# Performance work log

Measured on AMD Instinct MI355X. Metric: run time of the kernel, lower is better.

## Reference

```python
import jax, jax.numpy as jnp
import numpy as np

B, T, E = 2, 2048, 2048
H, H_KV, D = 16, 8, 128
THETA = 10000.0


def setup_inputs() -> dict:
    key = jax.random.key(0)
    ks = jax.random.split(key, 5)
    s = lambda n: (1.0 / np.sqrt(n))
    x = jax.random.normal(ks[0], (B, T, E), dtype=jnp.float32)
    wq = jax.random.normal(ks[1], (E, H * D), dtype=jnp.float32) * s(E)
    wk = jax.random.normal(ks[2], (E, H_KV * D), dtype=jnp.float32) * s(E)
    wv = jax.random.normal(ks[3], (E, H_KV * D), dtype=jnp.float32) * s(E)
    wo = jax.random.normal(ks[4], (H * D, E), dtype=jnp.float32) * s(H * D)
    # causal mask, broadcast over batch and heads
    mask = jnp.tril(jnp.ones((T, T), dtype=jnp.int32))[None, None, :, :]
    return {"x": x, "mask": mask, "wq": wq, "wk": wk, "wv": wv, "wo": wo}


def _rope(q, k):
    # q,k: [B,H,T,D]; deinterleave even/odd, rotate, concat halves (as in source)
    Tq, Dh = q.shape[2], q.shape[3] // 2
    inv = 1.0 / (THETA ** (jnp.arange(Dh, dtype=jnp.float32) / Dh))
    ang = jnp.arange(Tq, dtype=jnp.float32)[:, None] * inv[None, :]  # [T,Dh]
    c, s = jnp.cos(ang), jnp.sin(ang)  # broadcast over [B,H]
    q1, q2 = q[..., ::2], q[..., 1::2]
    k1, k2 = k[..., ::2], k[..., 1::2]
    q_rot = jnp.concatenate([q1 * c - q2 * s, q2 * c + q1 * s], axis=-1)
    k_rot = jnp.concatenate([k1 * c - k2 * s, k2 * c + k1 * s], axis=-1)
    return q_rot, k_rot


def reference(x, mask, wq, wk, wv, wo):
    Bx, Tx, _ = x.shape
    scale = D ** -0.5
    q = (x @ wq).reshape(Bx, Tx, H, D).transpose(0, 2, 1, 3)      # [B,H,T,D]
    k = (x @ wk).reshape(Bx, Tx, H_KV, D).transpose(0, 2, 1, 3)   # [B,Hkv,T,D]
    v = (x @ wv).reshape(Bx, Tx, H_KV, D).transpose(0, 2, 1, 3)
    # torch .repeat tiles along head axis: [kv0..kv7, kv0..kv7]
    k = jnp.tile(k, (1, H // H_KV, 1, 1))
    v = jnp.tile(v, (1, H // H_KV, 1, 1))
    q, k = _rope(q, k)
    attn = jnp.einsum('bhtd,bhsd->bhts', q, k) * scale
    attn = jnp.where(mask == 0, -jnp.inf, attn)
    w = jax.nn.softmax(attn, axis=-1)
    w = jnp.where(jnp.isnan(w), 0.0, w)
    out = jnp.einsum('bhts,bhsd->bhtd', w, v)
    out = out.transpose(0, 2, 1, 3).reshape(Bx, Tx, H * D)
    return out @ wo
```

## Files before the change

### kernel.cpp

```cpp
#include <hip/hip_runtime.h>
#include <hip/hip_bf16.h>
#include <cstdint>

typedef short bf16x8 __attribute__((ext_vector_type(8)));
typedef float f32x4 __attribute__((ext_vector_type(4)));
typedef unsigned short u16;
typedef unsigned int u32;

#define TT 2048

__device__ __forceinline__ u16 f2bf(float f) {
    __hip_bfloat16 h = __float2bfloat16(f);
    return __builtin_bit_cast(u16, h);
}
__device__ __forceinline__ float bf2f(u16 u) {
    return __builtin_bit_cast(float, (u32)u << 16);
}
__device__ __forceinline__ f32x4 mfma16(bf16x8 a, bf16x8 b, f32x4 c) {
    return __builtin_amdgcn_mfma_f32_16x16x32_bf16(a, b, c, 0, 0, 0);
}
__device__ __forceinline__ bf16x8 ldg8(const u16* p) {
    return __builtin_bit_cast(bf16x8, *reinterpret_cast<const uint4*>(p));
}
__device__ __forceinline__ bf16x8 lds8(const u16* p) {
    return *reinterpret_cast<const bf16x8*>(p);
}
__device__ __forceinline__ void gll16(const u16* g, u16* l) {
    __builtin_amdgcn_global_load_lds(
        (const __attribute__((address_space(1))) void*)g,
        (__attribute__((address_space(3))) void*)l, 16, 0, 0);
}

#define ASMBAR asm volatile("s_barrier" ::: "memory")
#define WAIT_VM8 asm volatile("s_waitcnt vmcnt(8)" ::: "memory")
#define WAIT_VM0 asm volatile("s_waitcnt vmcnt(0)" ::: "memory")
#define WAIT_LGKM0 asm volatile("s_waitcnt lgkmcnt(0)" ::: "memory")

__global__ __launch_bounds__(256) void prologue(const float* __restrict__ x,
                                                const float* __restrict__ wq,
                                                const float* __restrict__ wk,
                                                const float* __restrict__ wv,
                                                const float* __restrict__ wo,
                                                u16* __restrict__ xb,
                                                u16* __restrict__ wqkvT,
                                                u16* __restrict__ woT) {
    const int z = blockIdx.z;
    const int tid = threadIdx.x;
    if (z == 4) {
        int bix = blockIdx.y * 32 + blockIdx.x;
#pragma unroll
        for (int k = 0; k < 4; k++) {
            int idx = (bix * 1024 + k * 256 + tid) * 8;
            float4 a = *reinterpret_cast<const float4*>(&x[idx]);
            float4 b = *reinterpret_cast<const float4*>(&x[idx + 4]);
            u16 o[8] = {f2bf(a.x), f2bf(a.y), f2bf(a.z), f2bf(a.w),
                        f2bf(b.x), f2bf(b.y), f2bf(b.z), f2bf(b.w)};
            *reinterpret_cast<uint4*>(&xb[idx]) = *reinterpret_cast<const uint4*>(o);
        }
        return;
    }
    const float* src;
    u16* dst;
    int C, rope;
    const int R = 2048;
    if (z == 0) { src = wq; dst = wqkvT;               C = 2048; rope = 1; }
    else if (z == 1) { src = wk; dst = wqkvT + 2048 * 2048; C = 1024; rope = 1; }
    else if (z == 2) { src = wv; dst = wqkvT + 3072 * 2048; C = 1024; rope = 0; }
    else { src = wo; dst = woT;                        C = 2048; rope = 0; }
    const int cb = blockIdx.x, rb = blockIdx.y;
    if (cb * 64 >= C) return;

    __shared__ float tl[64][65];
#pragma unroll
    for (int i = 0; i < 16; i++) {
        int li = i * 256 + tid;
        int tr = li >> 6, tc = li & 63;
        tl[tr][tc] = src[(size_t)(rb * 64 + tr) * C + cb * 64 + tc];
    }
    __syncthreads();
#pragma unroll
    for (int i = 0; i < 16; i++) {
        int li = i * 256 + tid;
        int dr = li >> 6, dc = li & 63;
        int c = cb * 64 + dr;
        int j;
        if (rope) {
            int head = c >> 7, cl = c & 127, ii = cl >> 1, odd = cl & 1;
            j = head * 128 + ((ii & 15) | (odd << 4) | ((ii >> 4) << 5));
        } else {
            j = c;
        }
        dst[(size_t)j * R + rb * 64 + dc] = f2bf(tl[dc][dr]);
    }
}

template <int MODE>
__global__ __launch_bounds__(512, 2) void gemm256(const u16* __restrict__ A,
                                                  const u16* __restrict__ BT,
                                                  void* __restrict__ P0, void* __restrict__ P1,
                                                  void* __restrict__ P2, int M, int N, int K) {
    __shared__ __align__(16) u16 smA[2][256 * 64];
    __shared__ __align__(16) u16 smB[2][256 * 64];
    const int tid = threadIdx.x;
    const int w = tid >> 6, lane = tid & 63, quad = lane >> 4, l15 = lane & 15;
    const int wr = w >> 2, wc = w & 3;
    const int bm = blockIdx.y, bn = blockIdx.x;

    f32x4 acc[8][4];
    const f32x4 zf = {0.f, 0.f, 0.f, 0.f};
#pragma unroll
    for (int i = 0; i < 8; i++)
#pragma unroll
        for (int j = 0; j < 4; j++) acc[i][j] = zf;

    const u16* aSrc[4];
    const u16* bSrc[4];
#pragma unroll
    for (int i = 0; i < 4; i++) {
        int o = i * 512 + tid;
        int r = o >> 3, p = o & 7;
        int cc = p ^ (r & 7);
        aSrc[i] = A + (size_t)(bm * 256 + r) * K + cc * 8;
        bSrc[i] = BT + (size_t)(bn * 256 + r) * K + cc * 8;
    }
    auto stage = [&](int buf) {
#pragma unroll
        for (int i = 0; i < 4; i++) {
            gll16(aSrc[i], &smA[buf][(i * 512 + w * 64) * 8]);
            aSrc[i] += 64;
        }
#pragma unroll
        for (int i = 0; i < 4; i++) {
            gll16(bSrc[i], &smB[buf][(i * 512 + w * 64) * 8]);
            bSrc[i] += 64;
        }
    };

    stage(0);
    stage(1);
    WAIT_VM8;
    ASMBAR;

    const int nkt = K >> 6;
    for (int kt = 0; kt < nkt; ++kt) {
        const int cur = kt & 1;
        bf16x8 a[4][2], b01[2][2], b23[2][2];
#pragma unroll
        for (int mi = 0; mi < 4; mi++)
#pragma unroll
            for (int ks = 0; ks < 2; ks++) {
                int row = wr * 128 + mi * 16 + l15, cd = ks * 4 + quad;
                a[mi][ks] = lds8(&smA[cur][row * 64 + ((cd ^ (row & 7)) * 8)]);
            }
#pragma unroll
        for (int ni = 0; ni < 2; ni++)
#pragma unroll
            for (int ks = 0; ks < 2; ks++) {
                int row = wc * 64 + ni * 16 + l15, cd = ks * 4 + quad;
                b01[ni][ks] = lds8(&smB[cur][row * 64 + ((cd ^ (row & 7)) * 8)]);
            }
        ASMBAR;
        __builtin_amdgcn_s_setprio(1);
#pragma unroll
        for (int mi = 0; mi < 4; mi++)
#pragma unroll
            for (int ni = 0; ni < 2; ni++)
#pragma unroll
                for (int ks = 0; ks < 2; ks++)
                    acc[mi][ni] = mfma16(a[mi][ks], b01[ni][ks], acc[mi][ni]);
        __builtin_amdgcn_s_setprio(0);
        ASMBAR;
#pragma unroll
        for (int ni = 0; ni < 2; ni++)
#pragma unroll
            for (int ks = 0; ks < 2; ks++) {
                int row = wc * 64 + (ni + 2) * 16 + l15, cd = ks * 4 + quad;
                b23[ni][ks] = lds8(&smB[cur][row * 64 + ((cd ^ (row & 7)) * 8)]);
            }
        ASMBAR;
        __builtin_amdgcn_s_setprio(1);
#pragma unroll
        for (int mi = 0; mi < 4; mi++)
#pragma unroll
            for (int ni = 0; ni < 2; ni++)
#pragma unroll
                for (int ks = 0; ks < 2; ks++)
                    acc[mi][ni + 2] = mfma16(a[mi][ks], b23[ni][ks], acc[mi][ni + 2]);
        __builtin_amdgcn_s_setprio(0);
        ASMBAR;
#pragma unroll
        for (int mi = 0; mi < 4; mi++)
#pragma unroll
            for (int ks = 0; ks < 2; ks++) {
                int row = wr * 128 + (mi + 4) * 16 + l15, cd = ks * 4 + quad;
                a[mi][ks] = lds8(&smA[cur][row * 64 + ((cd ^ (row & 7)) * 8)]);
            }
        ASMBAR;
        __builtin_amdgcn_s_setprio(1);
#pragma unroll
        for (int mi = 0; mi < 4; mi++)
#pragma unroll
            for (int ni = 0; ni < 2; ni++)
#pragma unroll
                for (int ks = 0; ks < 2; ks++)
                    acc[mi + 4][ni + 2] = mfma16(a[mi][ks], b23[ni][ks], acc[mi + 4][ni + 2]);
        __builtin_amdgcn_s_setprio(0);
        WAIT_LGKM0;
        ASMBAR;
        if (kt + 2 < nkt) stage(cur);
        ASMBAR;
        __builtin_amdgcn_s_setprio(1);
#pragma unroll
        for (int mi = 0; mi < 4; mi++)
#pragma unroll
            for (int ni = 0; ni < 2; ni++)
#pragma unroll
                for (int ks = 0; ks < 2; ks++)
                    acc[mi + 4][ni] = mfma16(a[mi][ks], b01[ni][ks], acc[mi + 4][ni]);
        __builtin_amdgcn_s_setprio(0);
        if (kt + 2 < nkt) { WAIT_VM8; }
        else if (kt + 1 < nkt) { WAIT_VM0; }
        ASMBAR;
    }

    if (MODE == 1) {
#pragma unroll
        for (int mi = 0; mi < 8; mi++)
#pragma unroll
            for (int ni = 0; ni < 4; ni++)
#pragma unroll
                for (int r = 0; r < 4; r++) {
                    int m = bm * 256 + wr * 128 + mi * 16 + quad * 4 + r;
                    int n = bn * 256 + wc * 64 + ni * 16 + l15;
                    ((float*)P0)[(size_t)m * N + n] = acc[mi][ni][r];
                }
    } else if (bn < 12) {
#pragma unroll
        for (int mi = 0; mi < 8; mi++)
#pragma unroll
            for (int g = 0; g < 2; g++) {
                int i = ((wc & 1) * 2 + g) * 16 + l15;
                float inv = __expf(-0.14391156644f * (float)i);
#pragma unroll
                for (int r = 0; r < 4; r++) {
                    int m = bm * 256 + wr * 128 + mi * 16 + quad * 4 + r;
                    int b = m >> 11, t = m & 2047;
                    float ang = (float)t * inv;
                    float sn, cs;
                    __sincosf(ang, &sn, &cs);
                    float x1 = acc[mi][2 * g][r], x2 = acc[mi][2 * g + 1][r];
                    u16 o1 = f2bf(x1 * cs - x2 * sn);
                    u16 o2 = f2bf(x2 * cs + x1 * sn);
                    if (bn < 8) {
                        int h = bn * 2 + (wc >> 1);
                        u16* pq = (u16*)P0 + ((size_t)(b * 16 + h) * 2048 + t) * 128;
                        pq[i] = o1;
                        pq[i + 64] = o2;
                    } else {
                        int hk = (bn - 8) * 2 + (wc >> 1);
                        u16* pk = (u16*)P1 + ((size_t)(b * 8 + hk) * 2048 + t) * 128;
                        pk[i] = o1;
                        pk[i + 64] = o2;
                    }
                }
            }
    } else {
#pragma unroll
        for (int mi = 0; mi < 8; mi++)
#pragma unroll
            for (int ni = 0; ni < 4; ni++)
#pragma unroll
                for (int r = 0; r < 4; r++) {
                    int m = bm * 256 + wr * 128 + mi * 16 + quad * 4 + r;
                    int b = m >> 11, t = m & 2047;
                    int d = (wc & 1) * 64 + ni * 16 + l15;
                    int h = (bn - 12) * 2 + (wc >> 1);
                    ((u16*)P2)[((size_t)(b * 8 + h) * 128 + d) * 2048 + t] =
                        f2bf(acc[mi][ni][r]);
                }
    }
}

__global__ __launch_bounds__(256) void flash_attn(const u16* __restrict__ qg,
                                                  const u16* __restrict__ kg,
                                                  const u16* __restrict__ vg,
                                                  u16* __restrict__ og) {
    __shared__ __align__(16) u16 Ksm[2][64 * 128];
    __shared__ __align__(16) u16 Vsm[2][128 * 64];
    __shared__ __align__(16) u16 Pt[4 * 32 * 64];
    const int tid = threadIdx.x, w = tid >> 6, lane = tid & 63, quad = lane >> 4,
              l15 = lane & 15;
    const int bkv = blockIdx.x;
    const int qblk = 31 - (int)blockIdx.y;
    const int b = bkv >> 3, kvh = bkv & 7;
    const float scale = 0.08838834764831845f;

    const u16* kb = kg + (size_t)(b * 8 + kvh) * 2048 * 128;
    const u16* vb = vg + (size_t)(b * 8 + kvh) * 128 * 2048;

    bf16x8 aq[2][4];
#pragma unroll
    for (int hh = 0; hh < 2; hh++) {
        const int h = kvh + hh * 8;
        const u16* qp =
            qg + ((size_t)(b * 16 + h) * 2048 + qblk * 64 + w * 16 + l15) * 128 + quad * 8;
#pragma unroll
        for (int kk = 0; kk < 4; kk++) aq[hh][kk] = ldg8(qp + kk * 32);
    }

    f32x4 oacc[2][8];
    f32x4 lacc[2];
    const f32x4 zf = {0.f, 0.f, 0.f, 0.f};
#pragma unroll
    for (int hh = 0; hh < 2; hh++) {
        lacc[hh] = zf;
#pragma unroll
        for (int j = 0; j < 8; j++) oacc[hh][j] = zf;
    }
    bf16x8 ones;
#pragma unroll
    for (int i = 0; i < 8; i++) ones[i] = (short)0x3F80;

    auto stage = [&](int st, int buf) {
#pragma unroll
        for (int i = 0; i < 4; i++) {
            int o = i * 256 + w * 64 + lane;
            int s = o >> 4, p = o & 15;
            int cc = (p & 8) | ((p ^ s) & 7);
            gll16(kb + (size_t)(st * 64 + s) * 128 + cc * 8, &Ksm[buf][(i * 256 + w * 64) * 8]);
            int d = o >> 3, p2 = o & 7;
            int cc2 = (p2 ^ d) & 7;
            gll16(vb + (size_t)d * 2048 + st * 64 + cc2 * 8, &Vsm[buf][(i * 256 + w * 64) * 8]);
        }
    };

    stage(0, 0);
    for (int st = 0; st <= qblk; ++st) {
        const int cur = st & 1;
        __syncthreads();
        if (st < qblk) stage(st + 1, cur ^ 1);

        f32x4 s0[4], s1[4];
#pragma unroll
        for (int j = 0; j < 4; j++) {
            s0[j] = zf;
            s1[j] = zf;
#pragma unroll
            for (int kk = 0; kk < 4; kk++) {
                int srow = j * 16 + l15;
                int cd = kk * 4 + quad;
                int p = (cd & 8) | ((cd ^ srow) & 7);
                bf16x8 bk = lds8(&Ksm[cur][srow * 128 + p * 8]);
                s0[j] = mfma16(aq[0][kk], bk, s0[j]);
                s1[j] = mfma16(aq[1][kk], bk, s1[j]);
            }
        }
        const bool diag = (st == qblk);
#pragma unroll
        for (int j = 0; j < 4; j++)
#pragma unroll
            for (int r = 0; r < 4; r++) {
                bool masked = diag && (j * 16 + l15) > (w * 16 + quad * 4 + r);
                float p0 = masked ? 0.f : __expf(s0[j][r] * scale);
                float p1 = masked ? 0.f : __expf(s1[j][r] * scale);
                int prow = w * 32 + quad * 4 + r;
                int cc = (j * 2 + (l15 >> 3));
                int off = (l15 & 7);
                Pt[prow * 64 + ((cc ^ (prow & 7)) * 8) + off] = f2bf(p0);
                int prow1 = prow + 16;
                Pt[prow1 * 64 + ((cc ^ (prow1 & 7)) * 8) + off] = f2bf(p1);
            }
#pragma unroll
        for (int kk = 0; kk < 2; kk++) {
            int row0 = w * 32 + l15, row1 = row0 + 16;
            int cd2 = kk * 4 + quad;
            bf16x8 ap0 = lds8(&Pt[row0 * 64 + ((cd2 ^ (row0 & 7)) * 8)]);
            bf16x8 ap1 = lds8(&Pt[row1 * 64 + ((cd2 ^ (row1 & 7)) * 8)]);
#pragma unroll
            for (int jf = 0; jf < 8; jf++) {
                int drow = jf * 16 + l15;
                int p2 = (cd2 ^ drow) & 7;
                bf16x8 bv = lds8(&Vsm[cur][drow * 64 + p2 * 8]);
                oacc[0][jf] = mfma16(ap0, bv, oacc[0][jf]);
                oacc[1][jf] = mfma16(ap1, bv, oacc[1][jf]);
            }
            lacc[0] = mfma16(ap0, ones, lacc[0]);
            lacc[1] = mfma16(ap1, ones, lacc[1]);
        }
    }
#pragma unroll
    for (int hh = 0; hh < 2; hh++) {
        const int h = kvh + hh * 8;
#pragma unroll
        for (int jf = 0; jf < 8; jf++)
#pragma unroll
            for (int r = 0; r < 4; r++) {
                int t = qblk * 64 + w * 16 + quad * 4 + r;
                int d = jf * 16 + l15;
                og[((size_t)(b * 2048 + t) * 16 + h) * 128 + d] =
                    f2bf(oacc[hh][jf][r] / lacc[hh][r]);
            }
    }
}

extern "C" void kernel_launch(void* const* d_in, const int* in_sizes, int n_in, void* d_out,
                              int out_size, void* d_ws, size_t ws_size, hipStream_t stream) {
    const float* x = (const float*)d_in[0];
    const float* wq = (const float*)d_in[2];
    const float* wk = (const float*)d_in[3];
    const float* wv = (const float*)d_in[4];
    const float* wo = (const float*)d_in[5];
    float* out = (float*)d_out;

    char* ws = (char*)d_ws;
    u16* xb = (u16*)(ws);
    u16* wqkvT = (u16*)(ws + 16777216);
    u16* woT = (u16*)(ws + 33554432);
    u16* qbuf = (u16*)(ws + 41943040);
    u16* kbuf = (u16*)(ws + 58720256);
    u16* vtb = (u16*)(ws + 67108864);
    u16* obuf = xb;

    prologue<<<dim3(32, 32, 5), 256, 0, stream>>>(x, wq, wk, wv, wo, xb, wqkvT, woT);

    gemm256<0><<<dim3(16, 16), 512, 0, stream>>>(xb, wqkvT, qbuf, kbuf, vtb, 4096, 4096, 2048);

    flash_attn<<<dim3(16, 32), 256, 0, stream>>>(qbuf, kbuf, vtb, obuf);

    gemm256<1><<<dim3(8, 16), 512, 0, stream>>>(obuf, woT, out, nullptr, nullptr, 4096, 2048,
                                                2048);
}
```

Baseline: 341.5 us.

## Template GEMM on row-tile height and use 128-row tiles for output projection

Parameterizes the GEMM kernel on the number of M sub-tiles, so the output projection uses 128x256 tiles and launches 256 blocks instead of 128, filling more of the 256 CUs. The K-loop is also restructured: A and B staging are split and issued at different points in the MFMA sequence, the A fragment is loaded as low and high halves, and one barrier is removed. Smaller tiles cut per-block reuse of the B operand, and the new wait counts must match the number of in-flight loads.

Measured after the change: 323.0 us. 1.06x faster.

```diff
diff --git a/kernel.cpp b/kernel.cpp
--- a/kernel.cpp
+++ b/kernel.cpp
@@ -33,6 +33,7 @@
 
 #define ASMBAR asm volatile("s_barrier" ::: "memory")
 #define WAIT_VM8 asm volatile("s_waitcnt vmcnt(8)" ::: "memory")
+#define WAIT_VM6 asm volatile("s_waitcnt vmcnt(6)" ::: "memory")
 #define WAIT_VM0 asm volatile("s_waitcnt vmcnt(0)" ::: "memory")
 #define WAIT_LGKM0 asm volatile("s_waitcnt lgkmcnt(0)" ::: "memory")
 
@@ -94,41 +95,51 @@
     }
 }
 
-template <int MODE>
+template <int MODE, int MI>
 __global__ __launch_bounds__(512, 2) void gemm256(const u16* __restrict__ A,
                                                   const u16* __restrict__ BT,
                                                   void* __restrict__ P0, void* __restrict__ P1,
                                                   void* __restrict__ P2, int M, int N, int K) {
-    __shared__ __align__(16) u16 smA[2][256 * 64];
+    constexpr int BM = MI * 32;
+    constexpr int AR = MI / 2;
+    __shared__ __align__(16) u16 smA[2][BM * 64];
     __shared__ __align__(16) u16 smB[2][256 * 64];
     const int tid = threadIdx.x;
     const int w = tid >> 6, lane = tid & 63, quad = lane >> 4, l15 = lane & 15;
     const int wr = w >> 2, wc = w & 3;
     const int bm = blockIdx.y, bn = blockIdx.x;
 
-    f32x4 acc[8][4];
+    f32x4 acc[MI][4];
     const f32x4 zf = {0.f, 0.f, 0.f, 0.f};
 #pragma unroll
-    for (int i = 0; i < 8; i++)
+    for (int i = 0; i < MI; i++)
 #pragma unroll
         for (int j = 0; j < 4; j++) acc[i][j] = zf;
 
-    const u16* aSrc[4];
+    const u16* aSrc[AR];
     const u16* bSrc[4];
+#pragma unroll
+    for (int i = 0; i < AR; i++) {
+        int o = i * 512 + tid;
+        int r = o >> 3, p = o & 7;
+        int cc = p ^ (r & 7);
+        aSrc[i] = A + (size_t)(bm * BM + r) * K + cc * 8;
+    }
 #pragma unroll
     for (int i = 0; i < 4; i++) {
         int o = i * 512 + tid;
         int r = o >> 3, p = o & 7;
         int cc = p ^ (r & 7);
-        aSrc[i] = A + (size_t)(bm * 256 + r) * K + cc * 8;
         bSrc[i] = BT + (size_t)(bn * 256 + r) * K + cc * 8;
     }
-    auto stage = [&](int buf) {
-#pragma unroll
-        for (int i = 0; i < 4; i++) {
+    auto stageA = [&](int buf) {
+#pragma unroll
+        for (int i = 0; i < AR; i++) {
             gll16(aSrc[i], &smA[buf][(i * 512 + w * 64) * 8]);
             aSrc[i] += 64;
         }
+    };
+    auto stageB = [&](int buf) {
 #pragma unroll
         for (int i = 0; i < 4; i++) {
             gll16(bSrc[i], &smB[buf][(i * 512 + w * 64) * 8]);
@@ -136,21 +147,21 @@
         }
     };
 
-    stage(0);
-    stage(1);
-    WAIT_VM8;
+    stageA(0); stageB(0);
+    stageA(1); stageB(1);
+    if constexpr (MI == 8) { WAIT_VM8; } else { WAIT_VM6; }
     ASMBAR;
 
     const int nkt = K >> 6;
     for (int kt = 0; kt < nkt; ++kt) {
         const int cur = kt & 1;
-        bf16x8 a[4][2], b01[2][2], b23[2][2];
-#pragma unroll
-        for (int mi = 0; mi < 4; mi++)
+        bf16x8 aL[AR][2], aH[AR][2], b01[2][2], b23[2][2];
+#pragma unroll
+        for (int mi = 0; mi < AR; mi++)
 #pragma unroll
             for (int ks = 0; ks < 2; ks++) {
-                int row = wr * 128 + mi * 16 + l15, cd = ks * 4 + quad;
-                a[mi][ks] = lds8(&smA[cur][row * 64 + ((cd ^ (row & 7)) * 8)]);
+                int row = wr * (MI * 16) + mi * 16 + l15, cd = ks * 4 + quad;
+                aL[mi][ks] = lds8(&smA[cur][row * 64 + ((cd ^ (row & 7)) * 8)]);
             }
 #pragma unroll
         for (int ni = 0; ni < 2; ni++)
@@ -159,17 +170,6 @@
                 int row = wc * 64 + ni * 16 + l15, cd = ks * 4 + quad;
                 b01[ni][ks] = lds8(&smB[cur][row * 64 + ((cd ^ (row & 7)) * 8)]);
             }
-        ASMBAR;
-        __builtin_amdgcn_s_setprio(1);
-#pragma unroll
-        for (int mi = 0; mi < 4; mi++)
-#pragma unroll
-            for (int ni = 0; ni < 2; ni++)
-#pragma unroll
-                for (int ks = 0; ks < 2; ks++)
-                    acc[mi][ni] = mfma16(a[mi][ks], b01[ni][ks], acc[mi][ni]);
-        __builtin_amdgcn_s_setprio(0);
-        ASMBAR;
 #pragma unroll
         for (int ni = 0; ni < 2; ni++)
 #pragma unroll
@@ -180,70 +180,83 @@
         ASMBAR;
         __builtin_amdgcn_s_setprio(1);
 #pragma unroll
-        for (int mi = 0; mi < 4; mi++)
+        for (int mi = 0; mi < AR; mi++)
 #pragma unroll
             for (int ni = 0; ni < 2; ni++)
 #pragma unroll
                 for (int ks = 0; ks < 2; ks++)
-                    acc[mi][ni + 2] = mfma16(a[mi][ks], b23[ni][ks], acc[mi][ni + 2]);
+                    acc[mi][ni] = mfma16(aL[mi][ks], b01[ni][ks], acc[mi][ni]);
         __builtin_amdgcn_s_setprio(0);
         ASMBAR;
 #pragma unroll
-        for (int mi = 0; mi < 4; mi++)
+        for (int mi = 0; mi < AR; mi++)
 #pragma unroll
             for (int ks = 0; ks < 2; ks++) {
-                int row = wr * 128 + (mi + 4) * 16 + l15, cd = ks * 4 + quad;
-                a[mi][ks] = lds8(&smA[cur][row * 64 + ((cd ^ (row & 7)) * 8)]);
+                int row = wr * (MI * 16) + (mi + AR) * 16 + l15, cd = ks * 4 + quad;
+                aH[mi][ks] = lds8(&smA[cur][row * 64 + ((cd ^ (row & 7)) * 8)]);
             }
         ASMBAR;
         __builtin_amdgcn_s_setprio(1);
 #pragma unroll
-        for (int mi = 0; mi < 4; mi++)
+        for (int mi = 0; mi < AR; mi++)
 #pragma unroll
             for (int ni = 0; ni < 2; ni++)
 #pragma unroll
                 for (int ks = 0; ks < 2; ks++)
-                    acc[mi + 4][ni + 2] = mfma16(a[mi][ks], b23[ni][ks], acc[mi + 4][ni + 2]);
+                    acc[mi][ni + 2] = mfma16(aL[mi][ks], b23[ni][ks], acc[mi][ni + 2]);
         __builtin_amdgcn_s_setprio(0);
         WAIT_LGKM0;
         ASMBAR;
-        if (kt + 2 < nkt) stage(cur);
-        ASMBAR;
+        if (kt + 2 < nkt) stageA(cur);
         __builtin_amdgcn_s_setprio(1);
 #pragma unroll
-        for (int mi = 0; mi < 4; mi++)
+        for (int mi = 0; mi < AR; mi++)
 #pragma unroll
             for (int ni = 0; ni < 2; ni++)
 #pragma unroll
                 for (int ks = 0; ks < 2; ks++)
-                    acc[mi + 4][ni] = mfma16(a[mi][ks], b01[ni][ks], acc[mi + 4][ni]);
+                    acc[mi + AR][ni + 2] = mfma16(aH[mi][ks], b23[ni][ks], acc[mi + AR][ni + 2]);
         __builtin_amdgcn_s_setprio(0);
-        if (kt + 2 < nkt) { WAIT_VM8; }
-        else if (kt + 1 < nkt) { WAIT_VM0; }
+        ASMBAR;
+        if (kt + 2 < nkt) stageB(cur);
+        __builtin_amdgcn_s_setprio(1);
+#pragma unroll
+        for (int mi = 0; mi < AR; mi++)
+#pragma unroll
+            for (int ni = 0; ni < 2; ni++)
+#pragma unroll
+                for (int ks = 0; ks < 2; ks++)
+                    acc[mi + AR][ni] = mfma16(aH[mi][ks], b01[ni][ks], acc[mi + AR][ni]);
+        __builtin_amdgcn_s_setprio(0);
+        if (kt + 2 < nkt) {
+            if constexpr (MI == 8) { WAIT_VM8; } else { WAIT_VM6; }
+        } else if (kt + 1 < nkt) {
+            WAIT_VM0;
+        }
         ASMBAR;
     }
 
     if (MODE == 1) {
 #pragma unroll
-        for (int mi = 0; mi < 8; mi++)
+        for (int mi = 0; mi < MI; mi++)
 #pragma unroll
             for (int ni = 0; ni < 4; ni++)
 #pragma unroll
                 for (int r = 0; r < 4; r++) {
-                    int m = bm * 256 + wr * 128 + mi * 16 + quad * 4 + r;
+                    int m = bm * BM + wr * (MI * 16) + mi * 16 + quad * 4 + r;
                     int n = bn * 256 + wc * 64 + ni * 16 + l15;
                     ((float*)P0)[(size_t)m * N + n] = acc[mi][ni][r];
                 }
     } else if (bn < 12) {
 #pragma unroll
-        for (int mi = 0; mi < 8; mi++)
+        for (int mi = 0; mi < MI; mi++)
 #pragma unroll
             for (int g = 0; g < 2; g++) {
                 int i = ((wc & 1) * 2 + g) * 16 + l15;
                 float inv = __expf(-0.14391156644f * (float)i);
 #pragma unroll
                 for (int r = 0; r < 4; r++) {
-                    int m = bm * 256 + wr * 128 + mi * 16 + quad * 4 + r;
+                    int m = bm * BM + wr * (MI * 16) + mi * 16 + quad * 4 + r;
                     int b = m >> 11, t = m & 2047;
                     float ang = (float)t * inv;
                     float sn, cs;
@@ -266,12 +279,12 @@
             }
     } else {
 #pragma unroll
-        for (int mi = 0; mi < 8; mi++)
+        for (int mi = 0; mi < MI; mi++)
 #pragma unroll
             for (int ni = 0; ni < 4; ni++)
 #pragma unroll
                 for (int r = 0; r < 4; r++) {
-                    int m = bm * 256 + wr * 128 + mi * 16 + quad * 4 + r;
+                    int m = bm * BM + wr * (MI * 16) + mi * 16 + quad * 4 + r;
                     int b = m >> 11, t = m & 2047;
                     int d = (wc & 1) * 64 + ni * 16 + l15;
                     int h = (bn - 12) * 2 + (wc >> 1);
@@ -423,10 +436,11 @@
 
     prologue<<<dim3(32, 32, 5), 256, 0, stream>>>(x, wq, wk, wv, wo, xb, wqkvT, woT);
 
-    gemm256<0><<<dim3(16, 16), 512, 0, stream>>>(xb, wqkvT, qbuf, kbuf, vtb, 4096, 4096, 2048);
+    gemm256<0, 8><<<dim3(16, 16), 512, 0, stream>>>(xb, wqkvT, qbuf, kbuf, vtb, 4096, 4096,
+                                                    2048);
 
     flash_attn<<<dim3(16, 32), 256, 0, stream>>>(qbuf, kbuf, vtb, obuf);
 
-    gemm256<1><<<dim3(8, 16), 512, 0, stream>>>(obuf, woT, out, nullptr, nullptr, 4096, 2048,
-                                                2048);
-}
+    gemm256<1, 4><<<dim3(8, 32), 512, 0, stream>>>(obuf, woT, out, nullptr, nullptr, 4096,
+                                                   2048, 2048);
+}
```
